# Performance work log

Hardware: AMD Instinct MI355X
Metric: run time of the kernel (lower is better)

The kernel has to match this reference:

```python
import jax, jax.numpy as jnp
import numpy as np

B, N, E, D, STEPS = 32, 512, 4, 128, 5  # batch, n_node, n_edge_types, state_dim, n_steps


def setup_inputs() -> dict:
    key = jax.random.key(0)
    ks = jax.random.split(key, 16)
    s = 0.05  # xavier-ish scale for weights
    inp = {
        "prop_state": jax.random.normal(ks[0], (B, N, D), jnp.float32),
        # dense adjacency [B, N, 2*N*E]; scale by 1/(N) to keep bmm sums O(1)
        "A": jax.random.uniform(ks[1], (B, N, 2 * N * E), jnp.float32) * (2.0 / N),
        "node_mask": jnp.ones((B, N), dtype=jnp.int32),
        # per-edge-type in/out linears (applied orientation: x @ W + b)
        "in_W": jax.random.normal(ks[2], (E, D, D), jnp.float32) * s,
        "in_b": jax.random.normal(ks[3], (E, D), jnp.float32) * 1e-4,
        "out_W": jax.random.normal(ks[4], (E, D, D), jnp.float32) * s,
        "out_b": jax.random.normal(ks[5], (E, D), jnp.float32) * 1e-4,
        # GRU-style gates: Linear(3D -> D)
        "rW": jax.random.normal(ks[6], (3 * D, D), jnp.float32) * s,
        "rb": jax.random.normal(ks[7], (D,), jnp.float32) * 1e-4,
        "zW": jax.random.normal(ks[8], (3 * D, D), jnp.float32) * s,
        "zb": jax.random.normal(ks[9], (D,), jnp.float32) * 1e-4,
        "tW": jax.random.normal(ks[10], (3 * D, D), jnp.float32) * s,
        "tb": jax.random.normal(ks[11], (D,), jnp.float32) * 1e-4,
        # out_mlp: Linear(2D -> D) (dropout p=0 / eval mode -> identity)
        "oW": jax.random.normal(ks[12], (2 * D, D), jnp.float32) * s,
        "ob": jax.random.normal(ks[13], (D,), jnp.float32) * 1e-4,
    }
    return inp


def reference(prop_state, A, node_mask, in_W, in_b, out_W, out_b,
              rW, rb, zW, zb, tW, tb, oW, ob):
    del node_mask  # accepted but unused by GGNN.forward
    init_state = prop_state
    A_in = A[:, :, : N * E]    # [B, N, N*E]
    A_out = A[:, :, N * E:]    # [B, N, N*E]
    state = prop_state         # [B, N, D]
    for _ in range(STEPS):
        # per-edge-type linears, stacked edge-type-major: [B, E, N, D] -> [B, E*N, D]
        in_states = (jnp.einsum('bnd,edh->benh', state, in_W)
                     + in_b[None, :, None, :]).reshape(B, E * N, D)
        out_states = (jnp.einsum('bnd,edh->benh', state, out_W)
                      + out_b[None, :, None, :]).reshape(B, E * N, D)
        a_in = jnp.einsum('bnm,bmd->bnd', A_in, in_states)    # [B, N, D]
        a_out = jnp.einsum('bnm,bmd->bnd', A_out, out_states)  # [B, N, D]
        a = jnp.concatenate([a_in, a_out, state], axis=2)      # [B, N, 3D]
        r = jax.nn.sigmoid(a @ rW + rb)
        z = jax.nn.sigmoid(a @ zW + zb)
        joined = jnp.concatenate([a_in, a_out, r * state], axis=2)
        h_hat = jnp.tanh(joined @ tW + tb)
        state = (1.0 - z) * state + z * h_hat
    join_state = jnp.concatenate([state, init_state], axis=2)  # [B, N, 2D]
    return jnp.tanh(join_state @ oW + ob)                      # [B, N, D]
```

## Files before the change

kernel.cpp:

```cpp
#include <hip/hip_runtime.h>

#define DEV __device__ __forceinline__

using half8   = __attribute__((ext_vector_type(8))) _Float16;
using ushort8 = __attribute__((ext_vector_type(8))) unsigned short;
using f32x4   = __attribute__((ext_vector_type(4))) float;

typedef unsigned short ushort_t;

constexpr int B_ = 32, N_ = 512, E_ = 4, D_ = 128;
constexpr int NE = N_ * E_;
constexpr int M_TOT = B_ * N_;
constexpr int STEPS_ = 5;

DEV ushort_t f2h(float x) { union { _Float16 h; ushort_t u; } v; v.h = (_Float16)x; return v.u; }
DEV float sigmoidf_(float x) { return 1.0f / (1.0f + __expf(-x)); }

template<int ROWS>
DEV void stage64(const ushort_t* __restrict__ g, int ld, ushort_t* lds, int tid) {
    constexpr int TOT = ROWS * 8;
    static_assert(TOT % 256 == 0, "");
    int w = tid >> 6, lane = tid & 63;
#pragma unroll
    for (int c0 = 0; c0 < TOT; c0 += 256) {
        int c  = c0 + (w << 6) + lane;
        int r  = c >> 3;
        int cc = c & 7;
        __builtin_amdgcn_global_load_lds(
            (__attribute__((address_space(1))) void*)(g + r * ld + cc * 8),
            (__attribute__((address_space(3))) void*)(lds + (c0 + (w << 6)) * 8),
            16, 0, 0);
    }
}

DEV void st_swz(ushort_t* base, int row, int col, ushort_t v) {
    int off = ((row * 128 + col) * 2) ^ ((row & 7) << 4);
    *reinterpret_cast<ushort_t*>(reinterpret_cast<char*>(base) + off) = v;
}

template<int BM, int BN, int LDA, bool SWZ>
DEV void mmaT(const ushort_t* lA, int k0, const ushort_t* lB,
              f32x4 (&acc)[BM/32][BN/32], int wm, int wn, int l15, int lg) {
    constexpr int MF = BM/32, NF = BN/32;
#pragma unroll
    for (int kk = 0; kk < 2; ++kk) {
        half8 a[MF], b[NF];
#pragma unroll
        for (int i = 0; i < MF; ++i) {
            int row = wm*(BM/2) + i*16 + l15;
            int off = (row*LDA + k0 + kk*32 + lg*8) * 2;
            if (SWZ) off ^= (row & 7) << 4;
            a[i] = *reinterpret_cast<const half8*>(reinterpret_cast<const char*>(lA) + off);
        }
#pragma unroll
        for (int j = 0; j < NF; ++j)
            b[j] = *reinterpret_cast<const half8*>(lB + (wn*(BN/2)+j*16+l15)*64 + kk*32 + lg*8);
#pragma unroll
        for (int i = 0; i < MF; ++i)
#pragma unroll
            for (int j = 0; j < NF; ++j)
                acc[i][j] = __builtin_amdgcn_mfma_f32_16x16x32_f16(a[i], b[j], acc[i][j], 0, 0, 0);
    }
}

DEV void zacc(f32x4 (&acc)[2][4]) {
#pragma unroll
    for (int i = 0; i < 2; ++i)
#pragma unroll
        for (int j = 0; j < 4; ++j) acc[i][j] = (f32x4){0.f,0.f,0.f,0.f};
}

__global__ __launch_bounds__(256) void convertA_rs(const float* __restrict__ A,
                                                   ushort_t* __restrict__ A_h,
                                                   float* __restrict__ Ars) {
    int row = blockIdx.x, t = threadIdx.x;
    const float* src = A + (size_t)row * 4096 + t * 16;
    ushort_t* dst = A_h + (size_t)row * 4096 + t * 16;
    float s = 0.f;
#pragma unroll
    for (int c = 0; c < 2; ++c) {
        float4 v0 = reinterpret_cast<const float4*>(src)[2*c];
        float4 v1 = reinterpret_cast<const float4*>(src)[2*c+1];
        s += v0.x+v0.y+v0.z+v0.w + v1.x+v1.y+v1.z+v1.w;
        ushort8 r;
        r[0]=f2h(v0.x); r[1]=f2h(v0.y); r[2]=f2h(v0.z); r[3]=f2h(v0.w);
        r[4]=f2h(v1.x); r[5]=f2h(v1.y); r[6]=f2h(v1.z); r[7]=f2h(v1.w);
        *reinterpret_cast<ushort8*>(dst + 8*c) = r;
    }
#pragma unroll
    for (int m = 16; m; m >>= 1) s += __shfl_xor(s, m);
    if ((t & 31) == 0) Ars[(size_t)row * 8 + (t >> 5)] = s;
}

__global__ __launch_bounds__(256) void prep_weights(
    const float* __restrict__ in_W, const float* __restrict__ out_W,
    const float* __restrict__ rW, const float* __restrict__ zW,
    const float* __restrict__ tW, const float* __restrict__ oW,
    ushort_t* WstT, ushort_t* WrzT, ushort_t* WtT, ushort_t* WoT) {
    int idx = blockIdx.x * 256 + threadIdx.x;
    if (idx < 131072) {
        int io = idx >> 16, r = idx & 65535, d = r >> 9, eh = r & 511, e = eh >> 7, h = eh & 127;
        const float* W = io ? out_W : in_W;
        WstT[idx] = f2h(W[e*16384 + h*128 + d]);
        return;
    }
    idx -= 131072;
    if (idx < 98304) {
        int j = idx / 384, k = idx % 384;
        WrzT[idx] = f2h(j < 128 ? rW[k*128 + j] : zW[k*128 + (j-128)]);
        return;
    }
    idx -= 98304;
    if (idx < 49152) { int j = idx / 384, k = idx % 384; WtT[idx] = f2h(tW[k*128 + j]); return; }
    idx -= 49152;
    if (idx < 32768) { int j = idx / 256, k = idx % 256; WoT[idx] = f2h(oW[k*128 + j]); return; }
}

__global__ __launch_bounds__(256) void initPlus(const float* __restrict__ p,
                                                float* __restrict__ sf,
                                                ushort_t* __restrict__ sh,
                                                ushort_t* __restrict__ ih,
                                                ushort_t* __restrict__ stateT) {
    __shared__ ushort_t trb[128 * 132];
    int tid = threadIdx.x, mt = blockIdx.x;
    size_t base = (size_t)mt * 128 * 128;
#pragma unroll
    for (int rep = 0; rep < 16; ++rep) {
        int idx = rep * 256 + tid, row = idx >> 5, c4 = idx & 31;
        size_t o = base + (size_t)row * 128 + c4 * 4;
        float4 v = *reinterpret_cast<const float4*>(p + o);
        *reinterpret_cast<float4*>(sf + o) = v;
        using u4 = __attribute__((ext_vector_type(4))) unsigned short;
        u4 r; r[0]=f2h(v.x); r[1]=f2h(v.y); r[2]=f2h(v.z); r[3]=f2h(v.w);
        *reinterpret_cast<u4*>(sh + o) = r;
        *reinterpret_cast<u4*>(ih + o) = r;
        trb[row*132 + c4*4 + 0] = r[0]; trb[row*132 + c4*4 + 1] = r[1];
        trb[row*132 + c4*4 + 2] = r[2]; trb[row*132 + c4*4 + 3] = r[3];
    }
    __syncthreads();
    int b = mt >> 2, n0 = (mt & 3) * 128, d = tid >> 1, half = tid & 1;
    ushort_t* dst = stateT + (size_t)b * 65536 + (size_t)d * 512 + n0 + half * 64;
#pragma unroll
    for (int g2 = 0; g2 < 8; ++g2) {
        ushort8 v;
#pragma unroll
        for (int k = 0; k < 8; ++k) v[k] = trb[(half*64 + g2*8 + k)*132 + d];
        *reinterpret_cast<ushort8*>(dst + g2*8) = v;
    }
}

__global__ __launch_bounds__(256) void bigG_kernel(const ushort_t* __restrict__ A_h,
                                                   const ushort_t* __restrict__ stateT,
                                                   ushort_t* __restrict__ G) {
    __shared__ char smem[128*136*2] __attribute__((aligned(16)));
    ushort_t* sA  = (ushort_t*)smem;
    ushort_t* sB  = (ushort_t*)(smem + 16384);
    ushort_t* buf = (ushort_t*)smem;
    int tid = threadIdx.x, w = tid >> 6, l15 = tid & 15, lg = (tid & 63) >> 4;
    int wm = w >> 1, wn = w & 1;
    int bx = blockIdx.x;
    int bid = (bx & 7) * 128 + (bx >> 3);
    int nt = bid & 3, e = (bid >> 2) & 3, io = (bid >> 4) & 1, b = bid >> 5;

    const ushort_t* Asrc = A_h + ((size_t)(b*512 + nt*128))*4096 + io*2048 + e*512;
    const ushort_t* Bsrc = stateT + (size_t)b * 65536;
    ushort_t* Out = G + ((size_t)(b*512 + nt*128))*1024 + io*512 + e*128;

    f32x4 acc[4][4] = {};
    for (int k0 = 0; k0 < 512; k0 += 64) {
        stage64<128>(Asrc + k0, 4096, sA, tid);
        stage64<128>(Bsrc + k0, 512, sB, tid);
        __syncthreads();
        mmaT<128, 128, 64, false>(sA, 0, sB, acc, wm, wn, l15, lg);
        __syncthreads();
    }
#pragma unroll
    for (int j = 0; j < 4; ++j) {
        int col = wn*64 + j*16 + l15;
#pragma unroll
        for (int i = 0; i < 4; ++i)
#pragma unroll
            for (int q = 0; q < 4; ++q) {
                int row = wm*64 + i*16 + lg*4 + q;
                buf[row*136 + col] = f2h(acc[i][j][q]);
            }
    }
    __syncthreads();
#pragma unroll
    for (int rep = 0; rep < 8; ++rep) {
        int idx = rep*256 + tid, row = idx >> 4, c8 = idx & 15;
        uint4 v = *reinterpret_cast<uint4*>(buf + row*136 + c8*8);
        *reinterpret_cast<uint4*>(Out + (size_t)row*1024 + c8*8) = v;
    }
}

__global__ __launch_bounds__(256, 2) void gru_kernel(
    const ushort_t* __restrict__ G, const ushort_t* __restrict__ WstT,
    const float* __restrict__ Ars, const float* __restrict__ in_b,
    const float* __restrict__ out_b,
    const ushort_t* __restrict__ WrzT, const float* __restrict__ rb,
    const float* __restrict__ zb,
    const ushort_t* __restrict__ WtT, const float* __restrict__ tb,
    float* __restrict__ state_f32, ushort_t* __restrict__ state_h,
    ushort_t* __restrict__ stateT) {
    __shared__ char smem[73728] __attribute__((aligned(16)));
    ushort_t* sA    = (ushort_t*)smem;
    ushort_t* sB    = (ushort_t*)(smem + 8192);
    ushort_t* a_in  = (ushort_t*)(smem + 24576);
    ushort_t* a_out = (ushort_t*)(smem + 40960);
    ushort_t* rsb   = (ushort_t*)(smem + 57344);
    ushort_t* trb   = (ushort_t*)smem;

    int tid = threadIdx.x, w = tid >> 6, l15 = tid & 15, lg = (tid & 63) >> 4;
    int wm = w >> 1, wn = w & 1;
    int grow0 = blockIdx.x * 64;

    f32x4 acc[2][4];
    f32x4 zr[2][4];

#define GRU_KSTEP_GLB(APTR, ALD, BPTR, BLD) do {                         \
        stage64<64>((APTR), (ALD), sA, tid);                             \
        stage64<128>((BPTR), (BLD), sB, tid);                            \
        __syncthreads();                                                 \
        mmaT<64,128,64,false>(sA, 0, sB, acc, wm, wn, l15, lg);          \
        __syncthreads(); } while (0)

#define GRU_KSTEP_LDS(ABASE, K0, BPTR, BLD) do {                         \
        stage64<128>((BPTR), (BLD), sB, tid);                            \
        __syncthreads();                                                 \
        mmaT<64,128,128,true>((ABASE), (K0), sB, acc, wm, wn, l15, lg);  \
        __syncthreads(); } while (0)

    for (int io = 0; io < 2; ++io) {
        zacc(acc);
        for (int k0 = 0; k0 < 512; k0 += 64) {
            GRU_KSTEP_GLB(G + (size_t)grow0*1024 + io*512 + k0, 1024,
                          WstT + io*65536 + k0, 512);
        }
        const float* bio = io ? out_b : in_b;
        ushort_t* adst = io ? a_out : a_in;
#pragma unroll
        for (int j = 0; j < 4; ++j) {
            int col = wn*64 + j*16 + l15;
            float b0 = bio[col], b1 = bio[128+col], b2 = bio[256+col], b3 = bio[384+col];
#pragma unroll
            for (int i = 0; i < 2; ++i)
#pragma unroll
                for (int q = 0; q < 4; ++q) {
                    int row = wm*32 + i*16 + lg*4 + q;
                    float4 rsv = *reinterpret_cast<const float4*>(Ars + (size_t)(grow0+row)*8 + io*4);
                    float v = acc[i][j][q] + rsv.x*b0 + rsv.y*b1 + rsv.z*b2 + rsv.w*b3;
                    st_swz(adst, row, col, f2h(v));
                }
        }
    }

    zacc(acc);
    GRU_KSTEP_LDS(a_in,  0,  WrzT + 0,   384);
    GRU_KSTEP_LDS(a_in,  64, WrzT + 64,  384);
    GRU_KSTEP_LDS(a_out, 0,  WrzT + 128, 384);
    GRU_KSTEP_LDS(a_out, 64, WrzT + 192, 384);
    GRU_KSTEP_GLB(state_h + (size_t)grow0*128,      128, WrzT + 256, 384);
    GRU_KSTEP_GLB(state_h + (size_t)grow0*128 + 64, 128, WrzT + 320, 384);
#pragma unroll
    for (int j = 0; j < 4; ++j) {
        int col = wn*64 + j*16 + l15;
        float rbv = rb[col];
#pragma unroll
        for (int i = 0; i < 2; ++i)
#pragma unroll
            for (int q = 0; q < 4; ++q) {
                int row = wm*32 + i*16 + lg*4 + q;
                size_t idx = (size_t)(grow0+row)*128 + col;
                float rg = sigmoidf_(acc[i][j][q] + rbv);
                st_swz(rsb, row, col, f2h(rg * state_f32[idx]));
            }
    }

    zacc(acc);
    {
        const ushort_t* Wz = WrzT + 128*384;
        GRU_KSTEP_LDS(a_in,  0,  Wz + 0,   384);
        GRU_KSTEP_LDS(a_in,  64, Wz + 64,  384);
        GRU_KSTEP_LDS(a_out, 0,  Wz + 128, 384);
        GRU_KSTEP_LDS(a_out, 64, Wz + 192, 384);
        GRU_KSTEP_GLB(state_h + (size_t)grow0*128,      128, Wz + 256, 384);
        GRU_KSTEP_GLB(state_h + (size_t)grow0*128 + 64, 128, Wz + 320, 384);
    }
#pragma unroll
    for (int j = 0; j < 4; ++j) {
        int col = wn*64 + j*16 + l15;
        float zbv = zb[col];
#pragma unroll
        for (int i = 0; i < 2; ++i)
#pragma unroll
            for (int q = 0; q < 4; ++q)
                zr[i][j][q] = sigmoidf_(acc[i][j][q] + zbv);
    }

    zacc(acc);
    GRU_KSTEP_LDS(a_in,  0,  WtT + 0,   384);
    GRU_KSTEP_LDS(a_in,  64, WtT + 64,  384);
    GRU_KSTEP_LDS(a_out, 0,  WtT + 128, 384);
    GRU_KSTEP_LDS(a_out, 64, WtT + 192, 384);
    GRU_KSTEP_LDS(rsb,   0,  WtT + 256, 384);
    GRU_KSTEP_LDS(rsb,   64, WtT + 320, 384);
#pragma unroll
    for (int j = 0; j < 4; ++j) {
        int col = wn*64 + j*16 + l15;
        float tbv = tb[col];
#pragma unroll
        for (int i = 0; i < 2; ++i)
#pragma unroll
            for (int q = 0; q < 4; ++q) {
                int row = wm*32 + i*16 + lg*4 + q;
                size_t idx = (size_t)(grow0+row)*128 + col;
                float h = tanhf(acc[i][j][q] + tbv);
                float z = zr[i][j][q];
                float ns = (1.0f - z) * state_f32[idx] + z * h;
                state_f32[idx] = ns;
                trb[row*132 + col] = f2h(ns);
            }
    }
    __syncthreads();
#pragma unroll
    for (int rep = 0; rep < 4; ++rep) {
        int idx = rep*256 + tid, row = idx >> 4, c8 = idx & 15;
        ushort8 v;
#pragma unroll
        for (int k = 0; k < 8; ++k) v[k] = trb[row*132 + c8*8 + k];
        *reinterpret_cast<ushort8*>(state_h + (size_t)(grow0+row)*128 + c8*8) = v;
    }
    {
        int b = grow0 >> 9, n0 = grow0 & 511, d = tid >> 1, half = tid & 1;
        ushort_t* dst = stateT + (size_t)b*65536 + (size_t)d*512 + n0 + half*32;
#pragma unroll
        for (int g2 = 0; g2 < 4; ++g2) {
            ushort8 v;
#pragma unroll
            for (int k = 0; k < 8; ++k) v[k] = trb[(half*32 + g2*8 + k)*132 + d];
            *reinterpret_cast<ushort8*>(dst + g2*8) = v;
        }
    }
#undef GRU_KSTEP_GLB
#undef GRU_KSTEP_LDS
}

__global__ __launch_bounds__(256) void final_kernel(const ushort_t* __restrict__ state_h,
                                                    const ushort_t* __restrict__ init_h,
                                                    const ushort_t* __restrict__ WoT,
                                                    const float* __restrict__ ob,
                                                    float* __restrict__ out) {
    __shared__ alignas(16) ushort_t lA[128*64];
    __shared__ alignas(16) ushort_t lB[128*64];
    int tid = threadIdx.x, w = tid >> 6, l15 = tid & 15, lg = (tid & 63) >> 4;
    int wm = w >> 1, wn = w & 1;
    int mt = blockIdx.x;

    const ushort_t* srcs[2] = { state_h + (size_t)mt*128*128,
                                init_h + (size_t)mt*128*128 };
    f32x4 acc[4][4] = {};
    for (int k0 = 0; k0 < 256; k0 += 64) {
        stage64<128>(srcs[k0 >> 7] + (k0 & 127), 128, lA, tid);
        stage64<128>(WoT + k0, 256, lB, tid);
        __syncthreads();
        mmaT<128, 128, 64, false>(lA, 0, lB, acc, wm, wn, l15, lg);
        __syncthreads();
    }
#pragma unroll
    for (int j = 0; j < 4; ++j) {
        int col = wn*64 + j*16 + l15;
        float bv = ob[col];
#pragma unroll
        for (int i = 0; i < 4; ++i)
#pragma unroll
            for (int q = 0; q < 4; ++q) {
                int row = mt*128 + wm*64 + i*16 + lg*4 + q;
                out[(size_t)row * 128 + col] = tanhf(acc[i][j][q] + bv);
            }
    }
}

extern "C" void kernel_launch(void* const* d_in, const int* in_sizes, int n_in,
                              void* d_out, int out_size, void* d_ws, size_t ws_size,
                              hipStream_t stream) {
    const float* prop  = (const float*)d_in[0];
    const float* A     = (const float*)d_in[1];
    const float* in_W  = (const float*)d_in[3];
    const float* in_b  = (const float*)d_in[4];
    const float* out_W = (const float*)d_in[5];
    const float* out_b = (const float*)d_in[6];
    const float* rW    = (const float*)d_in[7];
    const float* rb    = (const float*)d_in[8];
    const float* zW    = (const float*)d_in[9];
    const float* zb    = (const float*)d_in[10];
    const float* tW    = (const float*)d_in[11];
    const float* tb    = (const float*)d_in[12];
    const float* oW    = (const float*)d_in[13];
    const float* ob    = (const float*)d_in[14];
    float* outp = (float*)d_out;

    size_t off = 0;
    auto carve = [&](size_t bytes) {
        void* p = (char*)d_ws + off;
        off += (bytes + 255) & ~(size_t)255;
        return p;
    };
    ushort_t* A_h      = (ushort_t*)carve((size_t)M_TOT*4096*2);
    ushort_t* G        = (ushort_t*)carve((size_t)M_TOT*1024*2);
    ushort_t* stateT   = (ushort_t*)carve((size_t)B_*D_*N_*2);
    ushort_t* state_h  = (ushort_t*)carve((size_t)M_TOT*D_*2);
    ushort_t* init_h   = (ushort_t*)carve((size_t)M_TOT*D_*2);
    float*    state_f32= (float*)carve((size_t)M_TOT*D_*4);
    float*    Ars      = (float*)carve((size_t)M_TOT*8*4);
    ushort_t* WstT     = (ushort_t*)carve((size_t)2*128*512*2);
    ushort_t* WrzT     = (ushort_t*)carve((size_t)256*384*2);
    ushort_t* WtT      = (ushort_t*)carve((size_t)128*384*2);
    ushort_t* WoT      = (ushort_t*)carve((size_t)128*256*2);
    (void)ws_size; (void)n_in; (void)in_sizes; (void)out_size;

    convertA_rs<<<16384, 256, 0, stream>>>(A, A_h, Ars);
    prep_weights<<<1216, 256, 0, stream>>>(in_W, out_W, rW, zW, tW, oW, WstT, WrzT, WtT, WoT);
    initPlus<<<128, 256, 0, stream>>>(prop, state_f32, state_h, init_h, stateT);

    for (int s = 0; s < STEPS_; ++s) {
        bigG_kernel<<<1024, 256, 0, stream>>>(A_h, stateT, G);
        gru_kernel<<<256, 256, 0, stream>>>(G, WstT, Ars, in_b, out_b,
                                            WrzT, rb, zb, WtT, tb,
                                            state_f32, state_h, stateT);
    }
    final_kernel<<<128, 256, 0, stream>>>(state_h, init_h, WoT, ob, outp);
}
```

Baseline: 832.2 us.

## Fuse adjacency bmm with edge-type projection and split GRU into row-tiled kernel

A new aio_kernel computes A·state for each edge type into a shared-memory tile, then immediately multiplies that tile by the matching edge-type weight slice and accumulates a_in or a_out. The 32 MB fp16 intermediate G no longer has to be written and read back on every step. The GRU gates move to a separate rzh_kernel that uses 32-row tiles, 512 blocks and less LDS, and keeps a_in, a_out and state resident in swizzled LDS. The cost is re-staging the state operand once per edge type and extra synchronisation per block.

```diff
diff --git a/kernel.cpp b/kernel.cpp
--- a/kernel.cpp
+++ b/kernel.cpp
@@ -63,11 +63,12 @@
     }
 }
 
-DEV void zacc(f32x4 (&acc)[2][4]) {
-#pragma unroll
-    for (int i = 0; i < 2; ++i)
-#pragma unroll
-        for (int j = 0; j < 4; ++j) acc[i][j] = (f32x4){0.f,0.f,0.f,0.f};
+template<int MF, int NF>
+DEV void zaccT(f32x4 (&a)[MF][NF]) {
+#pragma unroll
+    for (int i = 0; i < MF; ++i)
+#pragma unroll
+        for (int j = 0; j < NF; ++j) a[i][j] = (f32x4){0.f,0.f,0.f,0.f};
 }
 
 __global__ __launch_bounds__(256) void convertA_rs(const float* __restrict__ A,
@@ -149,201 +150,194 @@
     }
 }
 
-__global__ __launch_bounds__(256) void bigG_kernel(const ushort_t* __restrict__ A_h,
-                                                   const ushort_t* __restrict__ stateT,
-                                                   ushort_t* __restrict__ G) {
-    __shared__ char smem[128*136*2] __attribute__((aligned(16)));
-    ushort_t* sA  = (ushort_t*)smem;
-    ushort_t* sB  = (ushort_t*)(smem + 16384);
-    ushort_t* buf = (ushort_t*)smem;
+__global__ __launch_bounds__(256) void aio_kernel(
+    const ushort_t* __restrict__ A_h, const ushort_t* __restrict__ stateT,
+    const ushort_t* __restrict__ WstT, const float* __restrict__ Ars,
+    const float* __restrict__ in_b, const float* __restrict__ out_b,
+    ushort_t* __restrict__ a_in_h, ushort_t* __restrict__ a_out_h) {
+    __shared__ char smem[40960] __attribute__((aligned(16)));
+    ushort_t* sA     = (ushort_t*)smem;
+    ushort_t* sB     = (ushort_t*)(smem + 8192);
+    ushort_t* gseg   = (ushort_t*)(smem + 24576);
+    ushort_t* bounce = (ushort_t*)smem;
+
     int tid = threadIdx.x, w = tid >> 6, l15 = tid & 15, lg = (tid & 63) >> 4;
     int wm = w >> 1, wn = w & 1;
     int bx = blockIdx.x;
-    int bid = (bx & 7) * 128 + (bx >> 3);
-    int nt = bid & 3, e = (bid >> 2) & 3, io = (bid >> 4) & 1, b = bid >> 5;
-
-    const ushort_t* Asrc = A_h + ((size_t)(b*512 + nt*128))*4096 + io*2048 + e*512;
-    const ushort_t* Bsrc = stateT + (size_t)b * 65536;
-    ushort_t* Out = G + ((size_t)(b*512 + nt*128))*1024 + io*512 + e*128;
-
-    f32x4 acc[4][4] = {};
-    for (int k0 = 0; k0 < 512; k0 += 64) {
-        stage64<128>(Asrc + k0, 4096, sA, tid);
-        stage64<128>(Bsrc + k0, 512, sB, tid);
-        __syncthreads();
-        mmaT<128, 128, 64, false>(sA, 0, sB, acc, wm, wn, l15, lg);
-        __syncthreads();
-    }
-#pragma unroll
-    for (int j = 0; j < 4; ++j) {
-        int col = wn*64 + j*16 + l15;
-#pragma unroll
-        for (int i = 0; i < 4; ++i)
+    int bid = (bx & 7) * 64 + (bx >> 3);
+    int nt = bid & 7, io = (bid >> 3) & 1, b = bid >> 4;
+    int row0 = b * 512 + nt * 64;
+
+    const ushort_t* Abase = A_h + (size_t)row0 * 4096 + io * 2048;
+    const ushort_t* Bst   = stateT + (size_t)b * 65536;
+    const ushort_t* Wbase = WstT + io * 65536;
+
+    f32x4 acc_a[2][4]; zaccT(acc_a);
+    f32x4 accG[2][4];
+#pragma unroll 1
+    for (int e = 0; e < 4; ++e) {
+        zaccT(accG);
+        for (int k0 = 0; k0 < 512; k0 += 64) {
+            stage64<64>(Abase + e*512 + k0, 4096, sA, tid);
+            stage64<128>(Bst + k0, 512, sB, tid);
+            __syncthreads();
+            mmaT<64,128,64,false>(sA, 0, sB, accG, wm, wn, l15, lg);
+            __syncthreads();
+        }
+#pragma unroll
+        for (int j = 0; j < 4; ++j) {
+            int col = wn*64 + j*16 + l15;
+#pragma unroll
+            for (int i = 0; i < 2; ++i)
+#pragma unroll
+                for (int q = 0; q < 4; ++q)
+                    st_swz(gseg, wm*32 + i*16 + lg*4 + q, col, f2h(accG[i][j][q]));
+        }
+        for (int k0w = 0; k0w < 128; k0w += 64) {
+            stage64<128>(Wbase + e*128 + k0w, 512, sB, tid);
+            __syncthreads();
+            mmaT<64,128,128,true>(gseg, k0w, sB, acc_a, wm, wn, l15, lg);
+            __syncthreads();
+        }
+    }
+    const float* bio = io ? out_b : in_b;
+#pragma unroll
+    for (int j = 0; j < 4; ++j) {
+        int col = wn*64 + j*16 + l15;
+        float b0 = bio[col], b1 = bio[128+col], b2 = bio[256+col], b3 = bio[384+col];
+#pragma unroll
+        for (int i = 0; i < 2; ++i)
 #pragma unroll
             for (int q = 0; q < 4; ++q) {
-                int row = wm*64 + i*16 + lg*4 + q;
-                buf[row*136 + col] = f2h(acc[i][j][q]);
+                int row = wm*32 + i*16 + lg*4 + q;
+                float4 rsv = *reinterpret_cast<const float4*>(Ars + (size_t)(row0+row)*8 + io*4);
+                bounce[row*136 + col] =
+                    f2h(acc_a[i][j][q] + rsv.x*b0 + rsv.y*b1 + rsv.z*b2 + rsv.w*b3);
             }
     }
     __syncthreads();
-#pragma unroll
-    for (int rep = 0; rep < 8; ++rep) {
-        int idx = rep*256 + tid, row = idx >> 4, c8 = idx & 15;
-        uint4 v = *reinterpret_cast<uint4*>(buf + row*136 + c8*8);
-        *reinterpret_cast<uint4*>(Out + (size_t)row*1024 + c8*8) = v;
-    }
-}
-
-__global__ __launch_bounds__(256, 2) void gru_kernel(
-    const ushort_t* __restrict__ G, const ushort_t* __restrict__ WstT,
-    const float* __restrict__ Ars, const float* __restrict__ in_b,
-    const float* __restrict__ out_b,
+    ushort_t* adst = (io ? a_out_h : a_in_h) + (size_t)row0 * 128;
+#pragma unroll
+    for (int rep = 0; rep < 4; ++rep) {
+        int idx = rep*256 + tid, r = idx >> 4, c8 = idx & 15;
+        uint4 v = *reinterpret_cast<uint4*>(bounce + r*136 + c8*8);
+        *reinterpret_cast<uint4*>(adst + (size_t)r*128 + c8*8) = v;
+    }
+}
+
+__global__ __launch_bounds__(256) void rzh_kernel(
+    const ushort_t* __restrict__ a_in_h, const ushort_t* __restrict__ a_out_h,
+    const ushort_t* __restrict__ state_h_in,
     const ushort_t* __restrict__ WrzT, const float* __restrict__ rb,
     const float* __restrict__ zb,
     const ushort_t* __restrict__ WtT, const float* __restrict__ tb,
     float* __restrict__ state_f32, ushort_t* __restrict__ state_h,
     ushort_t* __restrict__ stateT) {
-    __shared__ char smem[73728] __attribute__((aligned(16)));
-    ushort_t* sA    = (ushort_t*)smem;
-    ushort_t* sB    = (ushort_t*)(smem + 8192);
-    ushort_t* a_in  = (ushort_t*)(smem + 24576);
-    ushort_t* a_out = (ushort_t*)(smem + 40960);
-    ushort_t* rsb   = (ushort_t*)(smem + 57344);
-    ushort_t* trb   = (ushort_t*)smem;
+    __shared__ char smem[40960] __attribute__((aligned(16)));
+    ushort_t* aT  = (ushort_t*)smem;
+    ushort_t* sB  = (ushort_t*)(smem + 24576);
+    ushort_t* trb = (ushort_t*)smem;
 
     int tid = threadIdx.x, w = tid >> 6, l15 = tid & 15, lg = (tid & 63) >> 4;
     int wm = w >> 1, wn = w & 1;
-    int grow0 = blockIdx.x * 64;
-
-    f32x4 acc[2][4];
-    f32x4 zr[2][4];
-
-#define GRU_KSTEP_GLB(APTR, ALD, BPTR, BLD) do {                         \
-        stage64<64>((APTR), (ALD), sA, tid);                             \
-        stage64<128>((BPTR), (BLD), sB, tid);                            \
-        __syncthreads();                                                 \
-        mmaT<64,128,64,false>(sA, 0, sB, acc, wm, wn, l15, lg);          \
+    int row0 = blockIdx.x * 32;
+
+    const ushort_t* base0 = a_in_h + (size_t)row0*128;
+    const ushort_t* base1 = a_out_h + (size_t)row0*128;
+    const ushort_t* base2 = state_h_in + (size_t)row0*128;
+#pragma unroll
+    for (int g0 = 0; g0 < 6; ++g0) {
+        int g = g0*256 + tid;
+        int T = g >> 9, r = (g >> 4) & 31, c = g & 15;
+        const ushort_t* bp = (T == 0) ? base0 : (T == 1) ? base1 : base2;
+        uint4 v = *reinterpret_cast<const uint4*>(bp + r*128 + c*8);
+        *reinterpret_cast<uint4*>(reinterpret_cast<char*>(aT) + T*8192 + r*256 + ((c ^ (r & 7)) << 4)) = v;
+    }
+
+    f32x4 acc[1][4];
+#define GSTEP(TS, K0W, BPTR) do {                                          \
+        stage64<128>((BPTR), 384, sB, tid);                                \
+        __syncthreads();                                                   \
+        mmaT<32,128,128,true>(aT + (TS)*4096, (K0W), sB, acc, wm, wn, l15, lg); \
         __syncthreads(); } while (0)
 
-#define GRU_KSTEP_LDS(ABASE, K0, BPTR, BLD) do {                         \
-        stage64<128>((BPTR), (BLD), sB, tid);                            \
-        __syncthreads();                                                 \
-        mmaT<64,128,128,true>((ABASE), (K0), sB, acc, wm, wn, l15, lg);  \
-        __syncthreads(); } while (0)
-
-    for (int io = 0; io < 2; ++io) {
-        zacc(acc);
-        for (int k0 = 0; k0 < 512; k0 += 64) {
-            GRU_KSTEP_GLB(G + (size_t)grow0*1024 + io*512 + k0, 1024,
-                          WstT + io*65536 + k0, 512);
-        }
-        const float* bio = io ? out_b : in_b;
-        ushort_t* adst = io ? a_out : a_in;
-#pragma unroll
-        for (int j = 0; j < 4; ++j) {
-            int col = wn*64 + j*16 + l15;
-            float b0 = bio[col], b1 = bio[128+col], b2 = bio[256+col], b3 = bio[384+col];
-#pragma unroll
-            for (int i = 0; i < 2; ++i)
-#pragma unroll
-                for (int q = 0; q < 4; ++q) {
-                    int row = wm*32 + i*16 + lg*4 + q;
-                    float4 rsv = *reinterpret_cast<const float4*>(Ars + (size_t)(grow0+row)*8 + io*4);
-                    float v = acc[i][j][q] + rsv.x*b0 + rsv.y*b1 + rsv.z*b2 + rsv.w*b3;
-                    st_swz(adst, row, col, f2h(v));
-                }
-        }
-    }
-
-    zacc(acc);
-    GRU_KSTEP_LDS(a_in,  0,  WrzT + 0,   384);
-    GRU_KSTEP_LDS(a_in,  64, WrzT + 64,  384);
-    GRU_KSTEP_LDS(a_out, 0,  WrzT + 128, 384);
-    GRU_KSTEP_LDS(a_out, 64, WrzT + 192, 384);
-    GRU_KSTEP_GLB(state_h + (size_t)grow0*128,      128, WrzT + 256, 384);
-    GRU_KSTEP_GLB(state_h + (size_t)grow0*128 + 64, 128, WrzT + 320, 384);
+    zaccT(acc);
+    GSTEP(0, 0,  WrzT + 0);   GSTEP(0, 64, WrzT + 64);
+    GSTEP(1, 0,  WrzT + 128); GSTEP(1, 64, WrzT + 192);
+    GSTEP(2, 0,  WrzT + 256); GSTEP(2, 64, WrzT + 320);
+    f32x4 rg[4];
 #pragma unroll
     for (int j = 0; j < 4; ++j) {
         int col = wn*64 + j*16 + l15;
         float rbv = rb[col];
 #pragma unroll
-        for (int i = 0; i < 2; ++i)
-#pragma unroll
-            for (int q = 0; q < 4; ++q) {
-                int row = wm*32 + i*16 + lg*4 + q;
-                size_t idx = (size_t)(grow0+row)*128 + col;
-                float rg = sigmoidf_(acc[i][j][q] + rbv);
-                st_swz(rsb, row, col, f2h(rg * state_f32[idx]));
-            }
-    }
-
-    zacc(acc);
+        for (int q = 0; q < 4; ++q) rg[j][q] = sigmoidf_(acc[0][j][q] + rbv);
+    }
+    zaccT(acc);
     {
         const ushort_t* Wz = WrzT + 128*384;
-        GRU_KSTEP_LDS(a_in,  0,  Wz + 0,   384);
-        GRU_KSTEP_LDS(a_in,  64, Wz + 64,  384);
-        GRU_KSTEP_LDS(a_out, 0,  Wz + 128, 384);
-        GRU_KSTEP_LDS(a_out, 64, Wz + 192, 384);
-        GRU_KSTEP_GLB(state_h + (size_t)grow0*128,      128, Wz + 256, 384);
-        GRU_KSTEP_GLB(state_h + (size_t)grow0*128 + 64, 128, Wz + 320, 384);
-    }
+        GSTEP(0, 0,  Wz + 0);   GSTEP(0, 64, Wz + 64);
+        GSTEP(1, 0,  Wz + 128); GSTEP(1, 64, Wz + 192);
+        GSTEP(2, 0,  Wz + 256); GSTEP(2, 64, Wz + 320);
+    }
+    f32x4 zg[4];
 #pragma unroll
     for (int j = 0; j < 4; ++j) {
         int col = wn*64 + j*16 + l15;
         float zbv = zb[col];
 #pragma unroll
-        for (int i = 0; i < 2; ++i)
-#pragma unroll
-            for (int q = 0; q < 4; ++q)
-                zr[i][j][q] = sigmoidf_(acc[i][j][q] + zbv);
-    }
-
-    zacc(acc);
-    GRU_KSTEP_LDS(a_in,  0,  WtT + 0,   384);
-    GRU_KSTEP_LDS(a_in,  64, WtT + 64,  384);
-    GRU_KSTEP_LDS(a_out, 0,  WtT + 128, 384);
-    GRU_KSTEP_LDS(a_out, 64, WtT + 192, 384);
-    GRU_KSTEP_LDS(rsb,   0,  WtT + 256, 384);
-    GRU_KSTEP_LDS(rsb,   64, WtT + 320, 384);
+        for (int q = 0; q < 4; ++q) zg[j][q] = sigmoidf_(acc[0][j][q] + zbv);
+    }
+#pragma unroll
+    for (int j = 0; j < 4; ++j) {
+        int col = wn*64 + j*16 + l15;
+#pragma unroll
+        for (int q = 0; q < 4; ++q) {
+            int row = wm*16 + lg*4 + q;
+            st_swz(aT + 2*4096, row, col,
+                   f2h(rg[j][q] * state_f32[(size_t)(row0+row)*128 + col]));
+        }
+    }
+    zaccT(acc);
+    GSTEP(0, 0,  WtT + 0);   GSTEP(0, 64, WtT + 64);
+    GSTEP(1, 0,  WtT + 128); GSTEP(1, 64, WtT + 192);
+    GSTEP(2, 0,  WtT + 256); GSTEP(2, 64, WtT + 320);
 #pragma unroll
     for (int j = 0; j < 4; ++j) {
         int col = wn*64 + j*16 + l15;
         float tbv = tb[col];
 #pragma unroll
-        for (int i = 0; i < 2; ++i)
-#pragma unroll
-            for (int q = 0; q < 4; ++q) {
-                int row = wm*32 + i*16 + lg*4 + q;
-                size_t idx = (size_t)(grow0+row)*128 + col;
-                float h = tanhf(acc[i][j][q] + tbv);
-                float z = zr[i][j][q];
-                float ns = (1.0f - z) * state_f32[idx] + z * h;
-                state_f32[idx] = ns;
-                trb[row*132 + col] = f2h(ns);
-            }
+        for (int q = 0; q < 4; ++q) {
+            int row = wm*16 + lg*4 + q;
+            size_t idx = (size_t)(row0+row)*128 + col;
+            float h = tanhf(acc[0][j][q] + tbv);
+            float z = zg[j][q];
+            float ns = (1.0f - z) * state_f32[idx] + z * h;
+            state_f32[idx] = ns;
+            trb[row*132 + col] = f2h(ns);
+        }
     }
     __syncthreads();
 #pragma unroll
-    for (int rep = 0; rep < 4; ++rep) {
-        int idx = rep*256 + tid, row = idx >> 4, c8 = idx & 15;
+    for (int rep = 0; rep < 2; ++rep) {
+        int idx = rep*256 + tid, r = idx >> 4, c8 = idx & 15;
         ushort8 v;
 #pragma unroll
-        for (int k = 0; k < 8; ++k) v[k] = trb[row*132 + c8*8 + k];
-        *reinterpret_cast<ushort8*>(state_h + (size_t)(grow0+row)*128 + c8*8) = v;
+        for (int k = 0; k < 8; ++k) v[k] = trb[r*132 + c8*8 + k];
+        *reinterpret_cast<ushort8*>(state_h + (size_t)(row0+r)*128 + c8*8) = v;
     }
     {
-        int b = grow0 >> 9, n0 = grow0 & 511, d = tid >> 1, half = tid & 1;
-        ushort_t* dst = stateT + (size_t)b*65536 + (size_t)d*512 + n0 + half*32;
-#pragma unroll
-        for (int g2 = 0; g2 < 4; ++g2) {
+        int b = row0 >> 9, n0 = row0 & 511, d = tid >> 1, half = tid & 1;
+        ushort_t* dst = stateT + (size_t)b*65536 + (size_t)d*512 + n0 + half*16;
+#pragma unroll
+        for (int g2 = 0; g2 < 2; ++g2) {
             ushort8 v;
 #pragma unroll
-            for (int k = 0; k < 8; ++k) v[k] = trb[(half*32 + g2*8 + k)*132 + d];
+            for (int k = 0; k < 8; ++k) v[k] = trb[(half*16 + g2*8 + k)*132 + d];
             *reinterpret_cast<ushort8*>(dst + g2*8) = v;
         }
     }
-#undef GRU_KSTEP_GLB
-#undef GRU_KSTEP_LDS
+#undef GSTEP
 }
 
 __global__ __launch_bounds__(256) void final_kernel(const ushort_t* __restrict__ state_h,
@@ -407,8 +401,9 @@
         return p;
     };
     ushort_t* A_h      = (ushort_t*)carve((size_t)M_TOT*4096*2);
-    ushort_t* G        = (ushort_t*)carve((size_t)M_TOT*1024*2);
     ushort_t* stateT   = (ushort_t*)carve((size_t)B_*D_*N_*2);
+    ushort_t* a_in_h   = (ushort_t*)carve((size_t)M_TOT*D_*2);
+    ushort_t* a_out_h  = (ushort_t*)carve((size_t)M_TOT*D_*2);
     ushort_t* state_h  = (ushort_t*)carve((size_t)M_TOT*D_*2);
     ushort_t* init_h   = (ushort_t*)carve((size_t)M_TOT*D_*2);
     float*    state_f32= (float*)carve((size_t)M_TOT*D_*4);
@@ -424,8 +419,9 @@
     initPlus<<<128, 256, 0, stream>>>(prop, state_f32, state_h, init_h, stateT);
 
     for (int s = 0; s < STEPS_; ++s) {
-        bigG_kernel<<<1024, 256, 0, stream>>>(A_h, stateT, G);
-        gru_kernel<<<256, 256, 0, stream>>>(G, WstT, Ars, in_b, out_b,
+        aio_kernel<<<512, 256, 0, stream>>>(A_h, stateT, WstT, Ars, in_b, out_b,
+                                            a_in_h, a_out_h);
+        rzh_kernel<<<512, 256, 0, stream>>>(a_in_h, a_out_h, state_h,
                                             WrzT, rb, zb, WtT, tb,
                                             state_f32, state_h, stateT);
     }
```

After: 830.5 us. About the same (-0.2%).
